# Kernel tuning notes

Hardware: AMD Instinct MI355X
Metric: run time of the kernel (lower is better)

Reference implementation:

```python
import jax, jax.numpy as jnp
import numpy as np
from jax import lax

B, N, F_, K, C = 16, 64, 1024, 13, 2   # batch, channels, feat(time), conv kernel, classes
EPS_BN = 1e-5


def setup_inputs() -> dict:
    key = jax.random.key(0)
    ks = jax.random.split(key, 12)
    kf = 1.0 / np.sqrt(F_)   # torch uniform init bound for Linear(F,.) and w
    kn = 1.0 / np.sqrt(N)    # Conv1d(N,1,k=1) bound
    kk = 1.0 / np.sqrt(K)    # Conv1d(1,1,k=K) bound
    u = lambda k, shape, b: jax.random.uniform(k, shape, jnp.float32, -b, b)
    return {
        "x": jax.random.normal(ks[0], (B, N, F_), jnp.float32),
        "w": u(ks[1], (F_,), kf),
        "gin_W": u(ks[2], (F_, F_), kf),
        "gin_b": u(ks[3], (F_,), kf),
        "bn1_g": jnp.ones((N,), jnp.float32),
        "bn1_b": jnp.zeros((N,), jnp.float32),
        "lc_W": u(ks[4], (N,), kn),
        "lc_b": u(ks[5], (1,), kn),
        "conv_W": u(ks[6], (1, 1, K), kk),
        "conv_b": u(ks[7], (1,), kk),
        "bn2_g": jnp.ones((1,), jnp.float32),
        "bn2_b": jnp.zeros((1,), jnp.float32),
        "out_W": u(ks[8], (C, F_), kf),
        "out_b": u(ks[9], (C,), kf),
    }


def reference(x, w, gin_W, gin_b, bn1_g, bn1_b, lc_W, lc_b, conv_W, conv_b,
              bn2_g, bn2_b, out_W, out_b):
    # --- learned adjacency: weighted L1 pairwise score ---
    diff = jnp.abs(x[:, :, None, :] - x[:, None, :, :])        # [B,N,N,F] big intermediate
    s = jnp.einsum('bijf,f->bij', diff, w)                      # [B,N,N]
    s = -jax.nn.relu(s)
    adj = jax.nn.softmax(s, axis=1)                             # softmax over dim 1 (as torch)
    # --- GIN aggregation (eps=0): (adj + I) @ x, then Linear ---
    a = adj + jnp.eye(N, dtype=x.dtype)
    h = jnp.einsum('bij,bjf->bif', a, x)                        # [B,N,F]
    h = jnp.einsum('bif,of->bio', h, gin_W) + gin_b             # [B,N,F]
    # --- BatchNorm1d over channels (train-mode batch stats, biased var) ---
    m = h.mean(axis=(0, 2), keepdims=True)
    v = h.var(axis=(0, 2), keepdims=True)
    h = (h - m) / jnp.sqrt(v + EPS_BN) * bn1_g[None, :, None] + bn1_b[None, :, None]
    # --- Conv1d(N->1, k=1): channel mixing ---
    y = jnp.einsum('bnf,n->bf', h, lc_W) + lc_b                 # [B,F]
    # --- Conv1d(1->1, k=K, padding='same') ---
    y = lax.conv_general_dilated(y[:, None, :], conv_W, (1,), 'SAME') + conv_b[None, :, None]
    # --- BatchNorm1d(1) ---
    m2 = y.mean(axis=(0, 2), keepdims=True)
    v2 = y.var(axis=(0, 2), keepdims=True)
    y = (y - m2) / jnp.sqrt(v2 + EPS_BN) * bn2_g[None, :, None] + bn2_b[None, :, None]
    # --- head ---
    y = jax.nn.relu(y.reshape(B, F_))
    logits = y @ out_W.T + out_b                                # [B,C]
    return jax.nn.softmax(logits, axis=1), adj
```

## Files before the change

kernel.cpp:

```cpp
#include <hip/hip_runtime.h>
#include <hip/hip_bf16.h>


typedef __attribute__((ext_vector_type(8))) __bf16 bf16x8;
typedef __attribute__((ext_vector_type(4))) float f32x4;

__device__ __forceinline__ unsigned short f2bf(float f) {
  union { float f; unsigned int u; } v; v.f = f;
  unsigned int r = v.u + 0x7FFFu + ((v.u >> 16) & 1u);
  return (unsigned short)(r >> 16);
}

__global__ __launch_bounds__(256) void k1_spart_gemm(
    const float* __restrict__ x, const float* __restrict__ w,
    const float* __restrict__ gin_W,
    float* __restrict__ spart, float* __restrict__ gpart) {
  __shared__ __align__(16) union {
    struct { float xt[64 * 68]; float wt[64]; } s;
    struct { unsigned short A[128 * 72]; unsigned short B[128 * 72]; } g;
  } sm;
  int t = threadIdx.x, bid = blockIdx.x;

  if (bid >= 128) {
    int sbid = bid - 128;
    int b = sbid >> 4, ft = sbid & 15, f0 = ft * 64;
    for (int c = 0; c < 16; ++c) {
      int idx = c * 256 + t;
      int n = idx >> 6, f = idx & 63;
      sm.s.xt[n * 68 + f] = x[b * 65536 + n * 1024 + f0 + f];
    }
    if (t < 64) sm.s.wt[t] = w[f0 + t];
    __syncthreads();
    int i0 = (t >> 4) * 4, j0 = (t & 15) * 4;
    float acc[4][4];
#pragma unroll
    for (int ii = 0; ii < 4; ++ii)
#pragma unroll
      for (int jj = 0; jj < 4; ++jj) acc[ii][jj] = 0.f;
    for (int f = 0; f < 64; f += 4) {
      float4 wv = *reinterpret_cast<const float4*>(&sm.s.wt[f]);
      float4 av[4], bv[4];
#pragma unroll
      for (int ii = 0; ii < 4; ++ii) av[ii] = *reinterpret_cast<const float4*>(&sm.s.xt[(i0 + ii) * 68 + f]);
#pragma unroll
      for (int jj = 0; jj < 4; ++jj) bv[jj] = *reinterpret_cast<const float4*>(&sm.s.xt[(j0 + jj) * 68 + f]);
#pragma unroll
      for (int ii = 0; ii < 4; ++ii)
#pragma unroll
        for (int jj = 0; jj < 4; ++jj) {
          acc[ii][jj] += fabsf(av[ii].x - bv[jj].x) * wv.x
                       + fabsf(av[ii].y - bv[jj].y) * wv.y
                       + fabsf(av[ii].z - bv[jj].z) * wv.z
                       + fabsf(av[ii].w - bv[jj].w) * wv.w;
        }
    }
    float* out = spart + (size_t)sbid * 4096;
#pragma unroll
    for (int ii = 0; ii < 4; ++ii)
#pragma unroll
      for (int jj = 0; jj < 4; ++jj)
        out[(i0 + ii) * 64 + (j0 + jj)] = acc[ii][jj];
    return;
  }

  int g = bid;
  int xcd = g & 7, idx = g >> 3;
  int lt = idx & 7, slice = idx >> 3;
  int tr = 2 * (xcd & 3) + (lt >> 2);
  int tc = 4 * (xcd >> 2) + (lt & 3);
  int k0 = slice * 512;
  int wave = t >> 6, lane = t & 63;
  int wr = (wave >> 1) * 64, wc = (wave & 1) * 64;
  int lrow = lane & 15, kg = lane >> 4;
  f32x4 acc[4][4];
#pragma unroll
  for (int mi = 0; mi < 4; ++mi)
#pragma unroll
    for (int nj = 0; nj < 4; ++nj) acc[mi][nj] = f32x4{0.f, 0.f, 0.f, 0.f};

  for (int chunk = 0; chunk < 8; ++chunk) {
    int kc = k0 + chunk * 64;
#pragma unroll
    for (int u = 0; u < 8; ++u) {
      int idx4 = u * 256 + t;
      int row = idx4 >> 4, kq = idx4 & 15;
      float4 va = *reinterpret_cast<const float4*>(&x[(size_t)(tr * 128 + row) * 1024 + kc + kq * 4]);
      ushort4 ua; ua.x = f2bf(va.x); ua.y = f2bf(va.y); ua.z = f2bf(va.z); ua.w = f2bf(va.w);
      *reinterpret_cast<ushort4*>(&sm.g.A[row * 72 + kq * 4]) = ua;
      float4 vb = *reinterpret_cast<const float4*>(&gin_W[(size_t)(tc * 128 + row) * 1024 + kc + kq * 4]);
      ushort4 ub; ub.x = f2bf(vb.x); ub.y = f2bf(vb.y); ub.z = f2bf(vb.z); ub.w = f2bf(vb.w);
      *reinterpret_cast<ushort4*>(&sm.g.B[row * 72 + kq * 4]) = ub;
    }
    __syncthreads();
#pragma unroll
    for (int ks = 0; ks < 2; ++ks) {
      bf16x8 af[4], bf_[4];
#pragma unroll
      for (int mi = 0; mi < 4; ++mi)
        af[mi] = *reinterpret_cast<const bf16x8*>(&sm.g.A[(wr + mi * 16 + lrow) * 72 + ks * 32 + kg * 8]);
#pragma unroll
      for (int nj = 0; nj < 4; ++nj)
        bf_[nj] = *reinterpret_cast<const bf16x8*>(&sm.g.B[(wc + nj * 16 + lrow) * 72 + ks * 32 + kg * 8]);
#pragma unroll
      for (int mi = 0; mi < 4; ++mi)
#pragma unroll
        for (int nj = 0; nj < 4; ++nj)
          acc[mi][nj] = __builtin_amdgcn_mfma_f32_16x16x32_bf16(af[mi], bf_[nj], acc[mi][nj], 0, 0, 0);
    }
    __syncthreads();
  }
  float* gp = gpart + (size_t)slice * (1024u * 1024u);
#pragma unroll
  for (int mi = 0; mi < 4; ++mi) {
    int row = tr * 128 + wr + mi * 16 + kg * 4;
#pragma unroll
    for (int nj = 0; nj < 4; ++nj) {
      int col = tc * 128 + wc + nj * 16 + lrow;
#pragma unroll
      for (int r = 0; r < 4; ++r)
        gp[(size_t)(row + r) * 1024 + col] = acc[mi][nj][r];
    }
  }
}

__global__ __launch_bounds__(256) void k2_adj_h2(
    const float* __restrict__ spart, const float* __restrict__ gpart,
    const float* __restrict__ gin_b,
    float* __restrict__ dout, float* __restrict__ h2, float* __restrict__ part) {
  __shared__ float adjs[64 * 65];
  __shared__ float csum[256];
  __shared__ float cinv[64];
  __shared__ __align__(16) float gt[64 * 68];
  int t = threadIdx.x, bid = blockIdx.x;
  int xcd = bid & 7, local = bid >> 3;
  int b = (xcd << 1) | (local & 1);
  int ft = local >> 1;
  int f0 = ft * 64;
  {
    int i = t >> 4, fl = (t & 15) * 4;
#pragma unroll
    for (int c = 0; c < 4; ++c) {
      int row = c * 16 + i;
      const float* base = gpart + (size_t)(b * 64 + row) * 1024 + f0 + fl;
      float4 s0 = *reinterpret_cast<const float4*>(base);
      float4 s1 = *reinterpret_cast<const float4*>(base + (1u << 20));
      float4 g4;
      g4.x = s0.x + s1.x; g4.y = s0.y + s1.y;
      g4.z = s0.z + s1.z; g4.w = s0.w + s1.w;
      *reinterpret_cast<float4*>(&gt[row * 68 + fl]) = g4;
    }
  }
  int jl = t & 63, q = t >> 6;
  float v[16];
#pragma unroll
  for (int r = 0; r < 16; ++r) v[r] = 0.f;
  for (int ft2 = 0; ft2 < 16; ++ft2) {
    const float* p = spart + (size_t)(b * 16 + ft2) * 4096 + jl;
#pragma unroll
    for (int r = 0; r < 16; ++r) v[r] += p[(q * 16 + r) * 64];
  }
  float partsum = 0.f;
#pragma unroll
  for (int r = 0; r < 16; ++r) {
    float e = expf(-fmaxf(v[r], 0.f));
    adjs[(q * 16 + r) * 65 + jl] = e;
    partsum += e;
  }
  csum[q * 64 + jl] = partsum;
  __syncthreads();
  if (t < 64)
    cinv[t] = 1.f / (csum[t] + csum[64 + t] + csum[128 + t] + csum[192 + t]);
  __syncthreads();
  float ci = cinv[jl];
  float* doutAdj = dout + 32 + (size_t)b * 4096;
#pragma unroll
  for (int r = 0; r < 16; ++r) {
    float a = adjs[(q * 16 + r) * 65 + jl] * ci;
    adjs[(q * 16 + r) * 65 + jl] = a;
    if (ft == 0) doutAdj[(q * 16 + r) * 64 + jl] = a;
  }
  __syncthreads();
  int i0 = (t >> 4) * 4, fl = (t & 15) * 4;
  float4 gbv = *reinterpret_cast<const float4*>(&gin_b[f0 + fl]);
  float4 acc4[4];
#pragma unroll
  for (int ii = 0; ii < 4; ++ii)
    acc4[ii] = *reinterpret_cast<const float4*>(&gt[(i0 + ii) * 68 + fl]);
  for (int j = 0; j < 64; ++j) {
    float4 gv = *reinterpret_cast<const float4*>(&gt[j * 68 + fl]);
#pragma unroll
    for (int ii = 0; ii < 4; ++ii) {
      float a = adjs[(i0 + ii) * 65 + j];
      acc4[ii].x += a * gv.x; acc4[ii].y += a * gv.y;
      acc4[ii].z += a * gv.z; acc4[ii].w += a * gv.w;
    }
  }
  float rs[4], rq[4];
#pragma unroll
  for (int ii = 0; ii < 4; ++ii) {
    acc4[ii].x += gbv.x; acc4[ii].y += gbv.y; acc4[ii].z += gbv.z; acc4[ii].w += gbv.w;
    *reinterpret_cast<float4*>(&h2[(size_t)(b * 64 + i0 + ii) * 1024 + f0 + fl]) = acc4[ii];
    rs[ii] = (acc4[ii].x + acc4[ii].y) + (acc4[ii].z + acc4[ii].w);
    rq[ii] = (acc4[ii].x * acc4[ii].x + acc4[ii].y * acc4[ii].y)
           + (acc4[ii].z * acc4[ii].z + acc4[ii].w * acc4[ii].w);
  }
#pragma unroll
  for (int m = 1; m < 16; m <<= 1) {
#pragma unroll
    for (int r = 0; r < 4; ++r) {
      rs[r] += __shfl_xor(rs[r], m, 64);
      rq[r] += __shfl_xor(rq[r], m, 64);
    }
  }
  if ((t & 15) == 0) {
    float* pp = part + (size_t)(b * 16 + ft) * 128;
#pragma unroll
    for (int r = 0; r < 4; ++r) {
      int n = i0 + r;
      pp[2 * n]     = rs[r];
      pp[2 * n + 1] = rq[r];
    }
  }
}

__global__ __launch_bounds__(256) void k3_y_head(
    const float* __restrict__ h2, const float* __restrict__ part,
    const float* __restrict__ lc_W, const float* __restrict__ lc_b,
    const float* __restrict__ bn1_g, const float* __restrict__ bn1_b,
    const float* __restrict__ conv_W, const float* __restrict__ conv_b,
    const float* __restrict__ bn2_g, const float* __restrict__ bn2_b,
    const float* __restrict__ out_W, const float* __restrict__ out_b,
    float* __restrict__ y2, float* __restrict__ bn2part,
    float* __restrict__ dout, unsigned* __restrict__ bar) {
  __shared__ float redp[2][128];
  __shared__ float cls[64], dds[64];
  __shared__ float yloc[268];
  __shared__ float red[256], red2[256];
  __shared__ float c0s;
  __shared__ unsigned tk;
  int t = threadIdx.x, bid = blockIdx.x;
  int b = ((bid & 7) << 1) | ((bid >> 3) & 1);
  int fq = bid >> 4;
  int f0 = fq * 256;
  {
    int k = t & 127, h = t >> 7;
    float s = 0.f;
    const float* pp = part + (size_t)h * 128 * 128 + k;
    for (int p = 0; p < 128; ++p) s += pp[(size_t)p * 128];
    redp[h][k] = s;
  }
  __syncthreads();
  if (t < 64) {
    float sum = redp[0][2 * t] + redp[1][2 * t];
    float sq  = redp[0][2 * t + 1] + redp[1][2 * t + 1];
    float m = sum * (1.f / 16384.f);
    float var = sq * (1.f / 16384.f) - m * m;
    float inv = 1.f / sqrtf(var + 1e-5f);
    float g = bn1_g[t], be = bn1_b[t], lw = lc_W[t];
    cls[t] = lw * g * inv;
    dds[t] = lw * (be - m * inv * g);
  }
  __syncthreads();
  if (t == 0) {
    float s = 0.f;
    for (int n = 0; n < 64; ++n) s += dds[n];
    c0s = s + lc_b[0];
  }
  __syncthreads();
  float c0 = c0s;
  for (int idx = t; idx < 268; idx += 256) {
    int f = f0 - 6 + idx;
    float acc = 0.f;
    if (f >= 0 && f < 1024) {
      acc = c0;
      const float* col = h2 + (size_t)(b * 64) * 1024 + f;
      for (int n = 0; n < 64; ++n) acc += cls[n] * col[(size_t)n * 1024];
    }
    yloc[idx] = acc;
  }
  __syncthreads();
  float cw[13];
#pragma unroll
  for (int k = 0; k < 13; ++k) cw[k] = conv_W[k];
  float vv = conv_b[0];
#pragma unroll
  for (int k = 0; k < 13; ++k) vv += yloc[t + k] * cw[k];
  y2[b * 1024 + f0 + t] = vv;
  red[t] = vv; red2[t] = vv * vv;
  __syncthreads();
  for (int off = 128; off > 0; off >>= 1) {
    if (t < off) { red[t] += red[t + off]; red2[t] += red2[t + off]; }
    __syncthreads();
  }
  if (t == 0) {
    int dchunk = b * 4 + fq;
    bn2part[2 * dchunk] = red[0]; bn2part[2 * dchunk + 1] = red2[0];
  }

  __syncthreads();
  if (t == 0) { __threadfence(); tk = atomicAdd(bar, 1u); }
  __syncthreads();
  if ((tk & 63u) != 63u) return;
  __threadfence();

  {
    float S = 0.f, S2 = 0.f;
    for (int i = 0; i < 64; ++i) { S += bn2part[2 * i]; S2 += bn2part[2 * i + 1]; }
    float m2 = S * (1.f / 16384.f);
    float inv2 = 1.f / sqrtf(S2 * (1.f / 16384.f) - m2 * m2 + 1e-5f);
    float g2 = bn2_g[0] * inv2, be2 = bn2_b[0];
    int hb = t >> 4, seg = t & 15;
    const float4* yv = reinterpret_cast<const float4*>(&y2[hb * 1024 + seg * 64]);
    const float4* w0 = reinterpret_cast<const float4*>(&out_W[seg * 64]);
    const float4* w1 = reinterpret_cast<const float4*>(&out_W[1024 + seg * 64]);
    float a0 = 0.f, a1 = 0.f;
#pragma unroll 4
    for (int u = 0; u < 16; ++u) {
      float4 y4 = yv[u], cc0 = w0[u], cc1 = w1[u];
      float vx = fmaxf((y4.x - m2) * g2 + be2, 0.f);
      float vy = fmaxf((y4.y - m2) * g2 + be2, 0.f);
      float vz = fmaxf((y4.z - m2) * g2 + be2, 0.f);
      float vw = fmaxf((y4.w - m2) * g2 + be2, 0.f);
      a0 += vx * cc0.x + vy * cc0.y + vz * cc0.z + vw * cc0.w;
      a1 += vx * cc1.x + vy * cc1.y + vz * cc1.z + vw * cc1.w;
    }
    red[t] = a0; red2[t] = a1;
    __syncthreads();
    for (int off = 8; off > 0; off >>= 1) {
      if (seg < off) { red[t] += red[t + off]; red2[t] += red2[t + off]; }
      __syncthreads();
    }
    if (seg == 0) {
      float l0 = red[t] + out_b[0], l1 = red2[t] + out_b[1];
      float mx = fmaxf(l0, l1);
      float e0 = expf(l0 - mx), e1 = expf(l1 - mx);
      float inv = 1.f / (e0 + e1);
      dout[hb * 2 + 0] = e0 * inv;
      dout[hb * 2 + 1] = e1 * inv;
    }
  }
}

extern "C" void kernel_launch(void* const* d_in, const int* in_sizes, int n_in,
                              void* d_out, int out_size, void* d_ws, size_t ws_size,
                              hipStream_t stream) {
  (void)in_sizes; (void)n_in; (void)out_size; (void)ws_size;
  const float* x      = (const float*)d_in[0];
  const float* w      = (const float*)d_in[1];
  const float* gin_W  = (const float*)d_in[2];
  const float* gin_b  = (const float*)d_in[3];
  const float* bn1_g  = (const float*)d_in[4];
  const float* bn1_b  = (const float*)d_in[5];
  const float* lc_W   = (const float*)d_in[6];
  const float* lc_b   = (const float*)d_in[7];
  const float* conv_W = (const float*)d_in[8];
  const float* conv_b = (const float*)d_in[9];
  const float* bn2_g  = (const float*)d_in[10];
  const float* bn2_b  = (const float*)d_in[11];
  const float* out_W  = (const float*)d_in[12];
  const float* out_b  = (const float*)d_in[13];
  float* dout = (float*)d_out;

  char* ws = (char*)d_ws;
  float* spart   = (float*)ws;
  float* h2      = (float*)(ws + (4u << 20));
  float* gpart   = (float*)(ws + (8u << 20));
  float* part    = (float*)(ws + (16u << 20));
  float* y2      = (float*)(ws + (16u << 20) + (128u << 10));
  float* bn2part = (float*)(ws + (16u << 20) + (192u << 10));
  unsigned* bar  = (unsigned*)(ws + (16u << 20) + (194u << 10));

  k1_spart_gemm<<<dim3(384), dim3(256), 0, stream>>>(x, w, gin_W, spart, gpart);
  k2_adj_h2    <<<dim3(256), dim3(256), 0, stream>>>(spart, gpart, gin_b, dout, h2, part);
  k3_y_head    <<<dim3(64),  dim3(256), 0, stream>>>(h2, part, lc_W, lc_b, bn1_g, bn1_b,
                                                     conv_W, conv_b, bn2_g, bn2_b, out_W, out_b,
                                                     y2, bn2part, dout, bar);
}
```

Measured before the change: 67.04 us.

## Fuse GIN linear GEMM into adjacency/aggregation kernel, dropping split-K partials

```diff
diff --git a/kernel.cpp b/kernel.cpp
--- a/kernel.cpp
+++ b/kernel.cpp
@@ -11,193 +11,154 @@
   return (unsigned short)(r >> 16);
 }
 
-__global__ __launch_bounds__(256) void k1_spart_gemm(
+__global__ __launch_bounds__(256) void k1_spart(
     const float* __restrict__ x, const float* __restrict__ w,
-    const float* __restrict__ gin_W,
-    float* __restrict__ spart, float* __restrict__ gpart) {
+    float* __restrict__ spart) {
+  __shared__ __align__(16) float xt[64 * 68];
+  __shared__ __align__(16) float wt[64];
+  int t = threadIdx.x, bid = blockIdx.x;
+  int b = bid >> 4, ft = bid & 15, f0 = ft * 64;
+  for (int c = 0; c < 16; ++c) {
+    int idx = c * 256 + t;
+    int n = idx >> 6, f = idx & 63;
+    xt[n * 68 + f] = x[b * 65536 + n * 1024 + f0 + f];
+  }
+  if (t < 64) wt[t] = w[f0 + t];
+  __syncthreads();
+  int i0 = (t >> 4) * 4, j0 = (t & 15) * 4;
+  float acc[4][4];
+#pragma unroll
+  for (int ii = 0; ii < 4; ++ii)
+#pragma unroll
+    for (int jj = 0; jj < 4; ++jj) acc[ii][jj] = 0.f;
+  for (int f = 0; f < 64; f += 4) {
+    float4 wv = *reinterpret_cast<const float4*>(&wt[f]);
+    float4 av[4], bv[4];
+#pragma unroll
+    for (int ii = 0; ii < 4; ++ii) av[ii] = *reinterpret_cast<const float4*>(&xt[(i0 + ii) * 68 + f]);
+#pragma unroll
+    for (int jj = 0; jj < 4; ++jj) bv[jj] = *reinterpret_cast<const float4*>(&xt[(j0 + jj) * 68 + f]);
+#pragma unroll
+    for (int ii = 0; ii < 4; ++ii)
+#pragma unroll
+      for (int jj = 0; jj < 4; ++jj) {
+        acc[ii][jj] += fabsf(av[ii].x - bv[jj].x) * wv.x
+                     + fabsf(av[ii].y - bv[jj].y) * wv.y
+                     + fabsf(av[ii].z - bv[jj].z) * wv.z
+                     + fabsf(av[ii].w - bv[jj].w) * wv.w;
+      }
+  }
+  float* out = spart + (size_t)bid * 4096;
+#pragma unroll
+  for (int ii = 0; ii < 4; ++ii)
+#pragma unroll
+    for (int jj = 0; jj < 4; ++jj)
+      out[(i0 + ii) * 64 + (j0 + jj)] = acc[ii][jj];
+}
+
+__global__ __launch_bounds__(512) void k2_gemm_adj_h2(
+    const float* __restrict__ x, const float* __restrict__ gin_W,
+    const float* __restrict__ spart, const float* __restrict__ gin_b,
+    float* __restrict__ dout, float* __restrict__ h2, float* __restrict__ part) {
+  __shared__ __align__(16) float gt[64 * 68];
   __shared__ __align__(16) union {
-    struct { float xt[64 * 68]; float wt[64]; } s;
-    struct { unsigned short A[128 * 72]; unsigned short B[128 * 72]; } g;
+    struct { unsigned short A4[4][64 * 72]; unsigned short B4[4][64 * 72]; } st;
+    struct { float adjs[64 * 65]; float csum[512]; float cinv[64]; } aj;
   } sm;
-  int t = threadIdx.x, bid = blockIdx.x;
-
-  if (bid >= 128) {
-    int sbid = bid - 128;
-    int b = sbid >> 4, ft = sbid & 15, f0 = ft * 64;
-    for (int c = 0; c < 16; ++c) {
-      int idx = c * 256 + t;
-      int n = idx >> 6, f = idx & 63;
-      sm.s.xt[n * 68 + f] = x[b * 65536 + n * 1024 + f0 + f];
-    }
-    if (t < 64) sm.s.wt[t] = w[f0 + t];
-    __syncthreads();
-    int i0 = (t >> 4) * 4, j0 = (t & 15) * 4;
-    float acc[4][4];
-#pragma unroll
-    for (int ii = 0; ii < 4; ++ii)
-#pragma unroll
-      for (int jj = 0; jj < 4; ++jj) acc[ii][jj] = 0.f;
-    for (int f = 0; f < 64; f += 4) {
-      float4 wv = *reinterpret_cast<const float4*>(&sm.s.wt[f]);
-      float4 av[4], bv[4];
-#pragma unroll
-      for (int ii = 0; ii < 4; ++ii) av[ii] = *reinterpret_cast<const float4*>(&sm.s.xt[(i0 + ii) * 68 + f]);
-#pragma unroll
-      for (int jj = 0; jj < 4; ++jj) bv[jj] = *reinterpret_cast<const float4*>(&sm.s.xt[(j0 + jj) * 68 + f]);
-#pragma unroll
-      for (int ii = 0; ii < 4; ++ii)
-#pragma unroll
-        for (int jj = 0; jj < 4; ++jj) {
-          acc[ii][jj] += fabsf(av[ii].x - bv[jj].x) * wv.x
-                       + fabsf(av[ii].y - bv[jj].y) * wv.y
-                       + fabsf(av[ii].z - bv[jj].z) * wv.z
-                       + fabsf(av[ii].w - bv[jj].w) * wv.w;
-        }
-    }
-    float* out = spart + (size_t)sbid * 4096;
-#pragma unroll
-    for (int ii = 0; ii < 4; ++ii)
-#pragma unroll
-      for (int jj = 0; jj < 4; ++jj)
-        out[(i0 + ii) * 64 + (j0 + jj)] = acc[ii][jj];
-    return;
-  }
-
-  int g = bid;
-  int xcd = g & 7, idx = g >> 3;
-  int lt = idx & 7, slice = idx >> 3;
-  int tr = 2 * (xcd & 3) + (lt >> 2);
-  int tc = 4 * (xcd >> 2) + (lt & 3);
-  int k0 = slice * 512;
-  int wave = t >> 6, lane = t & 63;
-  int wr = (wave >> 1) * 64, wc = (wave & 1) * 64;
-  int lrow = lane & 15, kg = lane >> 4;
-  f32x4 acc[4][4];
-#pragma unroll
-  for (int mi = 0; mi < 4; ++mi)
-#pragma unroll
-    for (int nj = 0; nj < 4; ++nj) acc[mi][nj] = f32x4{0.f, 0.f, 0.f, 0.f};
-
-  for (int chunk = 0; chunk < 8; ++chunk) {
-    int kc = k0 + chunk * 64;
-#pragma unroll
-    for (int u = 0; u < 8; ++u) {
-      int idx4 = u * 256 + t;
-      int row = idx4 >> 4, kq = idx4 & 15;
-      float4 va = *reinterpret_cast<const float4*>(&x[(size_t)(tr * 128 + row) * 1024 + kc + kq * 4]);
-      ushort4 ua; ua.x = f2bf(va.x); ua.y = f2bf(va.y); ua.z = f2bf(va.z); ua.w = f2bf(va.w);
-      *reinterpret_cast<ushort4*>(&sm.g.A[row * 72 + kq * 4]) = ua;
-      float4 vb = *reinterpret_cast<const float4*>(&gin_W[(size_t)(tc * 128 + row) * 1024 + kc + kq * 4]);
-      ushort4 ub; ub.x = f2bf(vb.x); ub.y = f2bf(vb.y); ub.z = f2bf(vb.z); ub.w = f2bf(vb.w);
-      *reinterpret_cast<ushort4*>(&sm.g.B[row * 72 + kq * 4]) = ub;
-    }
-    __syncthreads();
-#pragma unroll
-    for (int ks = 0; ks < 2; ++ks) {
-      bf16x8 af[4], bf_[4];
-#pragma unroll
-      for (int mi = 0; mi < 4; ++mi)
-        af[mi] = *reinterpret_cast<const bf16x8*>(&sm.g.A[(wr + mi * 16 + lrow) * 72 + ks * 32 + kg * 8]);
-#pragma unroll
-      for (int nj = 0; nj < 4; ++nj)
-        bf_[nj] = *reinterpret_cast<const bf16x8*>(&sm.g.B[(wc + nj * 16 + lrow) * 72 + ks * 32 + kg * 8]);
-#pragma unroll
-      for (int mi = 0; mi < 4; ++mi)
-#pragma unroll
-        for (int nj = 0; nj < 4; ++nj)
-          acc[mi][nj] = __builtin_amdgcn_mfma_f32_16x16x32_bf16(af[mi], bf_[nj], acc[mi][nj], 0, 0, 0);
-    }
-    __syncthreads();
-  }
-  float* gp = gpart + (size_t)slice * (1024u * 1024u);
-#pragma unroll
-  for (int mi = 0; mi < 4; ++mi) {
-    int row = tr * 128 + wr + mi * 16 + kg * 4;
-#pragma unroll
-    for (int nj = 0; nj < 4; ++nj) {
-      int col = tc * 128 + wc + nj * 16 + lrow;
-#pragma unroll
-      for (int r = 0; r < 4; ++r)
-        gp[(size_t)(row + r) * 1024 + col] = acc[mi][nj][r];
-    }
-  }
-}
-
-__global__ __launch_bounds__(256) void k2_adj_h2(
-    const float* __restrict__ spart, const float* __restrict__ gpart,
-    const float* __restrict__ gin_b,
-    float* __restrict__ dout, float* __restrict__ h2, float* __restrict__ part) {
-  __shared__ float adjs[64 * 65];
-  __shared__ float csum[256];
-  __shared__ float cinv[64];
-  __shared__ __align__(16) float gt[64 * 68];
   int t = threadIdx.x, bid = blockIdx.x;
   int xcd = bid & 7, local = bid >> 3;
   int b = (xcd << 1) | (local & 1);
   int ft = local >> 1;
   int f0 = ft * 64;
-  {
-    int i = t >> 4, fl = (t & 15) * 4;
-#pragma unroll
-    for (int c = 0; c < 4; ++c) {
-      int row = c * 16 + i;
-      const float* base = gpart + (size_t)(b * 64 + row) * 1024 + f0 + fl;
-      float4 s0 = *reinterpret_cast<const float4*>(base);
-      float4 s1 = *reinterpret_cast<const float4*>(base + (1u << 20));
-      float4 g4;
-      g4.x = s0.x + s1.x; g4.y = s0.y + s1.y;
-      g4.z = s0.z + s1.z; g4.w = s0.w + s1.w;
-      *reinterpret_cast<float4*>(&gt[row * 68 + fl]) = g4;
-    }
-  }
-  int jl = t & 63, q = t >> 6;
-  float v[16];
-#pragma unroll
-  for (int r = 0; r < 16; ++r) v[r] = 0.f;
+  int wave = t >> 6, lane = t & 63;
+  int wr = (wave & 3) * 16, wc = (wave >> 2) * 32;
+  int lrow = lane & 15, kg = lane >> 4;
+
+  f32x4 acc[2] = {{0.f,0.f,0.f,0.f},{0.f,0.f,0.f,0.f}};
+  for (int bc = 0; bc < 4; ++bc) {
+    int kc = bc * 256;
+#pragma unroll
+    for (int u = 0; u < 8; ++u) {
+      int idx4 = u * 512 + t;
+      int sub = idx4 >> 10, rem = idx4 & 1023;
+      int row = rem >> 4, kq = rem & 15;
+      float4 va = *reinterpret_cast<const float4*>(&x[(size_t)b * 65536 + row * 1024 + kc + sub * 64 + kq * 4]);
+      ushort4 ua; ua.x = f2bf(va.x); ua.y = f2bf(va.y); ua.z = f2bf(va.z); ua.w = f2bf(va.w);
+      *reinterpret_cast<ushort4*>(&sm.st.A4[sub][row * 72 + kq * 4]) = ua;
+      float4 vb = *reinterpret_cast<const float4*>(&gin_W[(size_t)(f0 + row) * 1024 + kc + sub * 64 + kq * 4]);
+      ushort4 ub; ub.x = f2bf(vb.x); ub.y = f2bf(vb.y); ub.z = f2bf(vb.z); ub.w = f2bf(vb.w);
+      *reinterpret_cast<ushort4*>(&sm.st.B4[sub][row * 72 + kq * 4]) = ub;
+    }
+    __syncthreads();
+#pragma unroll
+    for (int sub = 0; sub < 4; ++sub)
+#pragma unroll
+      for (int ks = 0; ks < 2; ++ks) {
+        bf16x8 a = *reinterpret_cast<const bf16x8*>(&sm.st.A4[sub][(wr + lrow) * 72 + ks * 32 + kg * 8]);
+#pragma unroll
+        for (int c = 0; c < 2; ++c) {
+          bf16x8 bb = *reinterpret_cast<const bf16x8*>(&sm.st.B4[sub][(wc + c * 16 + lrow) * 72 + ks * 32 + kg * 8]);
+          acc[c] = __builtin_amdgcn_mfma_f32_16x16x32_bf16(a, bb, acc[c], 0, 0, 0);
+        }
+      }
+    __syncthreads();
+  }
+#pragma unroll
+  for (int c = 0; c < 2; ++c)
+#pragma unroll
+    for (int r = 0; r < 4; ++r)
+      gt[(wr + kg * 4 + r) * 68 + wc + c * 16 + lrow] = acc[c][r];
+  __syncthreads();
+
+  int jl = t & 63, q = wave;
+  float v[8];
+#pragma unroll
+  for (int r = 0; r < 8; ++r) v[r] = 0.f;
   for (int ft2 = 0; ft2 < 16; ++ft2) {
     const float* p = spart + (size_t)(b * 16 + ft2) * 4096 + jl;
 #pragma unroll
-    for (int r = 0; r < 16; ++r) v[r] += p[(q * 16 + r) * 64];
+    for (int r = 0; r < 8; ++r) v[r] += p[(q * 8 + r) * 64];
   }
   float partsum = 0.f;
 #pragma unroll
-  for (int r = 0; r < 16; ++r) {
+  for (int r = 0; r < 8; ++r) {
     float e = expf(-fmaxf(v[r], 0.f));
-    adjs[(q * 16 + r) * 65 + jl] = e;
+    sm.aj.adjs[(q * 8 + r) * 65 + jl] = e;
     partsum += e;
   }
-  csum[q * 64 + jl] = partsum;
-  __syncthreads();
-  if (t < 64)
-    cinv[t] = 1.f / (csum[t] + csum[64 + t] + csum[128 + t] + csum[192 + t]);
-  __syncthreads();
-  float ci = cinv[jl];
+  sm.aj.csum[q * 64 + jl] = partsum;
+  __syncthreads();
+  if (t < 64) {
+    float s = 0.f;
+#pragma unroll
+    for (int g2 = 0; g2 < 8; ++g2) s += sm.aj.csum[g2 * 64 + t];
+    sm.aj.cinv[t] = 1.f / s;
+  }
+  __syncthreads();
+  float ci = sm.aj.cinv[jl];
   float* doutAdj = dout + 32 + (size_t)b * 4096;
 #pragma unroll
-  for (int r = 0; r < 16; ++r) {
-    float a = adjs[(q * 16 + r) * 65 + jl] * ci;
-    adjs[(q * 16 + r) * 65 + jl] = a;
-    if (ft == 0) doutAdj[(q * 16 + r) * 64 + jl] = a;
-  }
-  __syncthreads();
-  int i0 = (t >> 4) * 4, fl = (t & 15) * 4;
+  for (int r = 0; r < 8; ++r) {
+    float a = sm.aj.adjs[(q * 8 + r) * 65 + jl] * ci;
+    sm.aj.adjs[(q * 8 + r) * 65 + jl] = a;
+    if (ft == 0) doutAdj[(q * 8 + r) * 64 + jl] = a;
+  }
+  __syncthreads();
+
+  int i0 = (t >> 4) * 2, fl = (t & 15) * 4;
   float4 gbv = *reinterpret_cast<const float4*>(&gin_b[f0 + fl]);
-  float4 acc4[4];
-#pragma unroll
-  for (int ii = 0; ii < 4; ++ii)
-    acc4[ii] = *reinterpret_cast<const float4*>(&gt[(i0 + ii) * 68 + fl]);
+  float4 acc4[2];
+  acc4[0] = *reinterpret_cast<const float4*>(&gt[i0 * 68 + fl]);
+  acc4[1] = *reinterpret_cast<const float4*>(&gt[(i0 + 1) * 68 + fl]);
   for (int j = 0; j < 64; ++j) {
     float4 gv = *reinterpret_cast<const float4*>(&gt[j * 68 + fl]);
-#pragma unroll
-    for (int ii = 0; ii < 4; ++ii) {
-      float a = adjs[(i0 + ii) * 65 + j];
-      acc4[ii].x += a * gv.x; acc4[ii].y += a * gv.y;
-      acc4[ii].z += a * gv.z; acc4[ii].w += a * gv.w;
-    }
-  }
-  float rs[4], rq[4];
-#pragma unroll
-  for (int ii = 0; ii < 4; ++ii) {
+    float a0 = sm.aj.adjs[i0 * 65 + j], a1 = sm.aj.adjs[(i0 + 1) * 65 + j];
+    acc4[0].x += a0 * gv.x; acc4[0].y += a0 * gv.y; acc4[0].z += a0 * gv.z; acc4[0].w += a0 * gv.w;
+    acc4[1].x += a1 * gv.x; acc4[1].y += a1 * gv.y; acc4[1].z += a1 * gv.z; acc4[1].w += a1 * gv.w;
+  }
+  float rs[2], rq[2];
+#pragma unroll
+  for (int ii = 0; ii < 2; ++ii) {
     acc4[ii].x += gbv.x; acc4[ii].y += gbv.y; acc4[ii].z += gbv.z; acc4[ii].w += gbv.w;
     *reinterpret_cast<float4*>(&h2[(size_t)(b * 64 + i0 + ii) * 1024 + f0 + fl]) = acc4[ii];
     rs[ii] = (acc4[ii].x + acc4[ii].y) + (acc4[ii].z + acc4[ii].w);
@@ -207,7 +168,7 @@
 #pragma unroll
   for (int m = 1; m < 16; m <<= 1) {
 #pragma unroll
-    for (int r = 0; r < 4; ++r) {
+    for (int r = 0; r < 2; ++r) {
       rs[r] += __shfl_xor(rs[r], m, 64);
       rq[r] += __shfl_xor(rq[r], m, 64);
     }
@@ -215,7 +176,7 @@
   if ((t & 15) == 0) {
     float* pp = part + (size_t)(b * 16 + ft) * 128;
 #pragma unroll
-    for (int r = 0; r < 4; ++r) {
+    for (int r = 0; r < 2; ++r) {
       int n = i0 + r;
       pp[2 * n]     = rs[r];
       pp[2 * n + 1] = rq[r];
@@ -364,15 +325,14 @@
   char* ws = (char*)d_ws;
   float* spart   = (float*)ws;
   float* h2      = (float*)(ws + (4u << 20));
-  float* gpart   = (float*)(ws + (8u << 20));
-  float* part    = (float*)(ws + (16u << 20));
-  float* y2      = (float*)(ws + (16u << 20) + (128u << 10));
-  float* bn2part = (float*)(ws + (16u << 20) + (192u << 10));
-  unsigned* bar  = (unsigned*)(ws + (16u << 20) + (194u << 10));
-
-  k1_spart_gemm<<<dim3(384), dim3(256), 0, stream>>>(x, w, gin_W, spart, gpart);
-  k2_adj_h2    <<<dim3(256), dim3(256), 0, stream>>>(spart, gpart, gin_b, dout, h2, part);
-  k3_y_head    <<<dim3(64),  dim3(256), 0, stream>>>(h2, part, lc_W, lc_b, bn1_g, bn1_b,
-                                                     conv_W, conv_b, bn2_g, bn2_b, out_W, out_b,
-                                                     y2, bn2part, dout, bar);
-}
+  float* part    = (float*)(ws + (8u << 20));
+  float* y2      = (float*)(ws + (8u << 20) + (128u << 10));
+  float* bn2part = (float*)(ws + (8u << 20) + (192u << 10));
+  unsigned* bar  = (unsigned*)(ws + (8u << 20) + (194u << 10));
+
+  k1_spart      <<<dim3(256), dim3(256), 0, stream>>>(x, w, spart);
+  k2_gemm_adj_h2<<<dim3(256), dim3(512), 0, stream>>>(x, gin_W, spart, gin_b, dout, h2, part);
+  k3_y_head     <<<dim3(64),  dim3(256), 0, stream>>>(h2, part, lc_W, lc_b, bn1_g, bn1_b,
+                                                      conv_W, conv_b, bn2_g, bn2_b, out_W, out_b,
+                                                      y2, bn2part, dout, bar);
+}
```

Measured after the change: 68.15 us. No clear change (+1.7%).
